# Optimization experiments

Hardware: AMD Instinct MI355X
Metric: run time of the kernel (lower is better)

Reference implementation:

```python
import jax, jax.numpy as jnp
import numpy as np

H = 4096        # hidden_size
NH = 32         # num query heads
NKV = 8         # num kv heads
HD = H // NH    # head_dim = 128
T_PREV = 16383  # cached tokens; new token makes T = 16384
BASE = 10000.0


def _rope(x, pos):
    # x: [heads, head_dim]; interleaved even/odd RoPE at a single position
    d = x.shape[-1]
    inv_freq = 1.0 / (BASE ** (jnp.arange(0, d, 2, dtype=jnp.float32) / d))
    f = pos * inv_freq                      # [d/2]
    c, s = jnp.cos(f), jnp.sin(f)
    xe, xo = x[..., 0::2], x[..., 1::2]
    out = jnp.stack([xe * c - xo * s, xe * s + xo * c], axis=-1)
    return out.reshape(x.shape)


def setup_inputs() -> dict:
    key = jax.random.key(0)
    ks = jax.random.split(key, 7)
    w = 0.02  # weight scale for numerical stability
    return {
        "hidden": jax.random.normal(ks[0], (H,), jnp.float32),
        "k_cache": jax.random.normal(ks[1], (T_PREV, NKV, HD), jnp.float32),
        "v_cache": jax.random.normal(ks[2], (T_PREV, NKV, HD), jnp.float32),
        "Wq": jax.random.normal(ks[3], (H, H), jnp.float32) * w,
        "Wk": jax.random.normal(ks[4], (NKV * HD, H), jnp.float32) * w,
        "Wv": jax.random.normal(ks[5], (NKV * HD, H), jnp.float32) * w,
        "Wo": jax.random.normal(ks[6], (H, H), jnp.float32) * w,
        "position_id": T_PREV,
    }


def reference(hidden, k_cache, v_cache, Wq, Wk, Wv, Wo, position_id):
    pos = jnp.float32(position_id)
    # projections (nn.Linear: y = W @ x), single token
    q = (Wq @ hidden).reshape(NH, HD)
    k = (Wk @ hidden).reshape(NKV, HD)
    v = (Wv @ hidden).reshape(NKV, HD)
    # inline RoPE on new q and k
    q = _rope(q, pos)
    k = _rope(k, pos)
    # contiguous KV including the new token
    k_all = jnp.concatenate([k_cache, k[None]], axis=0)   # [T, NKV, HD]
    v_all = jnp.concatenate([v_cache, v[None]], axis=0)
    # GQA: repeat KV heads to match query heads
    rep = NH // NKV
    k_all = jnp.repeat(k_all, rep, axis=1)                 # [T, NH, HD]
    v_all = jnp.repeat(v_all, rep, axis=1)
    # single-query attention
    scores = jnp.einsum('hd,thd->ht', q, k_all) / jnp.sqrt(jnp.float32(HD))
    attn = jax.nn.softmax(scores, axis=-1)                 # [NH, T]
    ctx = jnp.einsum('ht,thd->hd', attn, v_all)            # [NH, HD]
    # combine heads + output projection
    return Wo @ ctx.reshape(H)
```

## Files before the change

### kernel.cpp

```cpp
#include <hip/hip_runtime.h>
#include <math.h>

#define NH 32
#define NKV 8
#define HD 128
#define HDIM 4096
#define KVDIM 1024
#define TPREV 16383
#define NCHUNK 64
#define CHUNK 256

#define OFF_Q 0
#define OFF_K 4096
#define OFF_V 5120
#define OFF_PART 6144
#define PART_STRIDE 130
#define OFF_CTX (OFF_PART + NH * NCHUNK * PART_STRIDE)

__device__ __forceinline__ float wave_reduce_sum(float v) {
#pragma unroll
  for (int m = 32; m >= 1; m >>= 1) v += __shfl_xor(v, m, 64);
  return v;
}
__device__ __forceinline__ float wave_reduce_max(float v) {
#pragma unroll
  for (int m = 32; m >= 1; m >>= 1) v = fmaxf(v, __shfl_xor(v, m, 64));
  return v;
}
__device__ __forceinline__ float dot4(float4 a, float4 b) {
  return a.x * b.x + a.y * b.y + a.z * b.z + a.w * b.w;
}

__global__ __launch_bounds__(256) void qkv_rope_kernel(
    const float* __restrict__ Wq, const float* __restrict__ Wk,
    const float* __restrict__ Wv, const float* __restrict__ hidden,
    const int* __restrict__ pos_p, float* __restrict__ ws) {
  int r = blockIdx.x * 4 + (threadIdx.x >> 6);
  int lane = threadIdx.x & 63;
  const float* W;
  int wr;
  if (r < HDIM) {
    W = Wq; wr = r;
  } else if (r < HDIM + KVDIM) {
    W = Wk; wr = r - HDIM;
  } else {
    W = Wv; wr = r - HDIM - KVDIM;
  }
  const float4* w4 = (const float4*)(W + (size_t)wr * HDIM);
  const float4* h4 = (const float4*)hidden;
  float s = 0.f;
#pragma unroll
  for (int base = 0; base < 16; base += 8) {
    float4 a[8], b[8];
#pragma unroll
    for (int j = 0; j < 8; ++j) a[j] = w4[lane + 64 * (base + j)];
#pragma unroll
    for (int j = 0; j < 8; ++j) b[j] = h4[lane + 64 * (base + j)];
#pragma unroll
    for (int j = 0; j < 8; ++j) s += dot4(a[j], b[j]);
  }
  s = wave_reduce_sum(s);
  __shared__ float rs[4];
  if (lane == 0) rs[threadIdx.x >> 6] = s;
  __syncthreads();
  if (threadIdx.x < 2) {
    int r0 = blockIdx.x * 4 + (int)threadIdx.x * 2;
    float S0 = rs[threadIdx.x * 2], S1 = rs[threadIdx.x * 2 + 1];
    if (r0 < HDIM + KVDIM) {
      int j = (r0 & (HD - 1)) >> 1;
      double f = (double)(*pos_p) * pow(10000.0, -(double)j / 64.0);
      float c = (float)cos(f), sn = (float)sin(f);
      ws[r0] = S0 * c - S1 * sn;
      ws[r0 + 1] = S0 * sn + S1 * c;
    } else {
      ws[r0] = S0;
      ws[r0 + 1] = S1;
    }
  }
}

__global__ __launch_bounds__(256, 2) void attn_chunk_kernel(
    const float* __restrict__ k_cache, const float* __restrict__ v_cache,
    float* __restrict__ ws) {
  int g = blockIdx.x >> 6;
  int c = blockIdx.x & 63;
  int t0 = c * CHUNK;
  int tid = threadIdx.x;

  __shared__ float qs[4 * HD];
  __shared__ float sc[CHUNK * 5];
  __shared__ float vacc[8][4][HD];
  __shared__ float wredm[4][4], wredl[4][4];
  __shared__ float mh[4], lh[4];

  for (int i = tid; i < 4 * HD; i += 256) qs[i] = ws[OFF_Q + g * 4 * HD + i];
  __syncthreads();

  const float rscale = 0.08838834764831845f;

  int tok = t0 + tid;
  bool valid = tok < TPREV;
  float s0 = -1e30f, s1 = -1e30f, s2 = -1e30f, s3 = -1e30f;
  if (valid) {
    const float4* kp = (const float4*)(k_cache + (size_t)tok * KVDIM + g * HD);
    const float4* q4 = (const float4*)qs;
    s0 = 0.f; s1 = 0.f; s2 = 0.f; s3 = 0.f;
#pragma unroll
    for (int base = 0; base < 32; base += 8) {
      float4 kk[8];
#pragma unroll
      for (int j = 0; j < 8; ++j) kk[j] = kp[base + j];
#pragma unroll
      for (int j = 0; j < 8; ++j) {
        s0 += dot4(kk[j], q4[0 * 32 + base + j]);
        s1 += dot4(kk[j], q4[1 * 32 + base + j]);
        s2 += dot4(kk[j], q4[2 * 32 + base + j]);
        s3 += dot4(kk[j], q4[3 * 32 + base + j]);
      }
    }
    s0 *= rscale; s1 *= rscale; s2 *= rscale; s3 *= rscale;
  }

  float m0 = wave_reduce_max(s0), m1 = wave_reduce_max(s1);
  float m2 = wave_reduce_max(s2), m3 = wave_reduce_max(s3);
  if ((tid & 63) == 0) {
    int w = tid >> 6;
    wredm[w][0] = m0; wredm[w][1] = m1; wredm[w][2] = m2; wredm[w][3] = m3;
  }
  __syncthreads();
  if (tid < 4)
    mh[tid] = fmaxf(fmaxf(wredm[0][tid], wredm[1][tid]),
                    fmaxf(wredm[2][tid], wredm[3][tid]));
  __syncthreads();

  float e0 = expf(s0 - mh[0]), e1 = expf(s1 - mh[1]);
  float e2 = expf(s2 - mh[2]), e3 = expf(s3 - mh[3]);
  sc[tid * 5 + 0] = e0;
  sc[tid * 5 + 1] = e1;
  sc[tid * 5 + 2] = e2;
  sc[tid * 5 + 3] = e3;
  float l0 = wave_reduce_sum(e0), l1 = wave_reduce_sum(e1);
  float l2 = wave_reduce_sum(e2), l3 = wave_reduce_sum(e3);
  if ((tid & 63) == 0) {
    int w = tid >> 6;
    wredl[w][0] = l0; wredl[w][1] = l1; wredl[w][2] = l2; wredl[w][3] = l3;
  }
  __syncthreads();
  if (tid < 4)
    lh[tid] = wredl[0][tid] + wredl[1][tid] + wredl[2][tid] + wredl[3][tid];
  __syncthreads();

  int grp = tid >> 5, lane = tid & 31;
  float4 a0 = {0, 0, 0, 0}, a1 = {0, 0, 0, 0}, a2 = {0, 0, 0, 0},
         a3 = {0, 0, 0, 0};
  const float4 z4 = {0, 0, 0, 0};
#pragma unroll
  for (int base = 0; base < 32; base += 4) {
    float4 vv[4];
#pragma unroll
    for (int j = 0; j < 4; ++j) {
      int it = grp + 8 * (base + j);
      int t = t0 + it;
      vv[j] = (t < TPREV)
                  ? ((const float4*)(v_cache + (size_t)t * KVDIM + g * HD))[lane]
                  : z4;
    }
#pragma unroll
    for (int j = 0; j < 4; ++j) {
      int it = grp + 8 * (base + j);
      float p0 = sc[it * 5 + 0], p1 = sc[it * 5 + 1];
      float p2 = sc[it * 5 + 2], p3 = sc[it * 5 + 3];
      a0.x = fmaf(p0, vv[j].x, a0.x); a0.y = fmaf(p0, vv[j].y, a0.y);
      a0.z = fmaf(p0, vv[j].z, a0.z); a0.w = fmaf(p0, vv[j].w, a0.w);
      a1.x = fmaf(p1, vv[j].x, a1.x); a1.y = fmaf(p1, vv[j].y, a1.y);
      a1.z = fmaf(p1, vv[j].z, a1.z); a1.w = fmaf(p1, vv[j].w, a1.w);
      a2.x = fmaf(p2, vv[j].x, a2.x); a2.y = fmaf(p2, vv[j].y, a2.y);
      a2.z = fmaf(p2, vv[j].z, a2.z); a2.w = fmaf(p2, vv[j].w, a2.w);
      a3.x = fmaf(p3, vv[j].x, a3.x); a3.y = fmaf(p3, vv[j].y, a3.y);
      a3.z = fmaf(p3, vv[j].z, a3.z); a3.w = fmaf(p3, vv[j].w, a3.w);
    }
  }
  ((float4*)&vacc[grp][0][0])[lane] = a0;
  ((float4*)&vacc[grp][1][0])[lane] = a1;
  ((float4*)&vacc[grp][2][0])[lane] = a2;
  ((float4*)&vacc[grp][3][0])[lane] = a3;
  __syncthreads();

  float* part = ws + OFF_PART;
#pragma unroll
  for (int rep = 0; rep < 2; ++rep) {
    int p = tid + rep * 256;
    int h = p >> 7, d = p & 127;
    float s = 0.f;
#pragma unroll
    for (int g2 = 0; g2 < 8; ++g2) s += vacc[g2][h][d];
    part[(size_t)((g * 4 + h) * NCHUNK + c) * PART_STRIDE + d] = s;
  }
  if (tid < 4) {
    part[(size_t)((g * 4 + tid) * NCHUNK + c) * PART_STRIDE + 128] = mh[tid];
    part[(size_t)((g * 4 + tid) * NCHUNK + c) * PART_STRIDE + 129] = lh[tid];
  }
}

__global__ __launch_bounds__(256) void combine_kernel(float* __restrict__ ws) {
  int h = blockIdx.x;
  int g = h >> 2;
  int tid = threadIdx.x;
  const float rscale = 0.08838834764831845f;
  const float* ph = ws + OFF_PART + (size_t)h * NCHUNK * PART_STRIDE;

  __shared__ float red[HD];
  __shared__ float wexp[NCHUNK];
  __shared__ float Msh, Lsh;
  __shared__ float acc2[HD];

  if (tid < HD) red[tid] = ws[OFF_Q + h * HD + tid] * ws[OFF_K + g * HD + tid];
  __syncthreads();
#pragma unroll
  for (int s2 = 64; s2 >= 1; s2 >>= 1) {
    if (tid < s2 && tid + s2 < HD) red[tid] += red[tid + s2];
    __syncthreads();
  }
  float snew = red[0] * rscale;

  if (tid < 64) {
    float m = ph[tid * PART_STRIDE + 128];
    float M = wave_reduce_max(fmaxf(m, snew));
    float w = expf(m - M);
    float lp = ph[tid * PART_STRIDE + 129] * w;
    float L = wave_reduce_sum(lp);
    wexp[tid] = w;
    if (tid == 0) { Msh = M; Lsh = L; }
  }
  __syncthreads();
  float M = Msh;
  float en = expf(snew - M);
  float L = Lsh + en;

  int half = tid >> 7, d = tid & 127;
  float acc = 0.f;
  int cbeg = half * 32;
#pragma unroll 8
  for (int c2 = cbeg; c2 < cbeg + 32; ++c2)
    acc = fmaf(ph[(size_t)c2 * PART_STRIDE + d], wexp[c2], acc);
  if (half == 0) acc2[d] = acc;
  __syncthreads();
  if (half == 1) acc2[d] += acc;
  __syncthreads();
  if (tid < HD)
    ws[OFF_CTX + h * HD + tid] =
        (acc2[tid] + en * ws[OFF_V + g * HD + tid]) / L;
}

__global__ __launch_bounds__(256) void out_matvec_kernel(
    const float* __restrict__ Wo, const float* __restrict__ ws,
    float* __restrict__ out) {
  int r = blockIdx.x * 4 + (threadIdx.x >> 6);
  int lane = threadIdx.x & 63;
  const float4* w4 = (const float4*)(Wo + (size_t)r * HDIM);
  const float4* x4 = (const float4*)(ws + OFF_CTX);
  float s = 0.f;
#pragma unroll
  for (int base = 0; base < 16; base += 8) {
    float4 a[8], b[8];
#pragma unroll
    for (int j = 0; j < 8; ++j) a[j] = w4[lane + 64 * (base + j)];
#pragma unroll
    for (int j = 0; j < 8; ++j) b[j] = x4[lane + 64 * (base + j)];
#pragma unroll
    for (int j = 0; j < 8; ++j) s += dot4(a[j], b[j]);
  }
  s = wave_reduce_sum(s);
  if (lane == 0) out[r] = s;
}

extern "C" void kernel_launch(void* const* d_in, const int* in_sizes, int n_in,
                              void* d_out, int out_size, void* d_ws,
                              size_t ws_size, hipStream_t stream) {
  const float* hidden = (const float*)d_in[0];
  const float* k_cache = (const float*)d_in[1];
  const float* v_cache = (const float*)d_in[2];
  const float* Wq = (const float*)d_in[3];
  const float* Wk = (const float*)d_in[4];
  const float* Wv = (const float*)d_in[5];
  const float* Wo = (const float*)d_in[6];
  const int* pos = (const int*)d_in[7];
  float* out = (float*)d_out;
  float* ws = (float*)d_ws;

  qkv_rope_kernel<<<(HDIM + 2 * KVDIM) / 4, 256, 0, stream>>>(Wq, Wk, Wv,
                                                              hidden, pos, ws);
  attn_chunk_kernel<<<NKV * NCHUNK, 256, 0, stream>>>(k_cache, v_cache, ws);
  combine_kernel<<<NH, 256, 0, stream>>>(ws);
  out_matvec_kernel<<<HDIM / 4, 256, 0, stream>>>(Wo, ws, out);
}
```

Measured before the change: 286.8 us.

## Halve attention chunk size, split K dot across thread pairs, cheapen RoPE trig

Doubles the number of attention chunks (128 tokens each), so the grid covers more CUs. Each K row's dot product is now split across two threads that combine with a lane shuffle. Occupancy is raised via launch bounds, and the combine kernel is generalised to reduce 128 partials across four waves. The RoPE frequency computation replaces double pow/cos/sin with a bitwise product of precomputed powers plus range reduction and float sincos. In exchange, the partials workspace and the combine kernel's work both double.

```diff
diff --git a/kernel.cpp b/kernel.cpp
--- a/kernel.cpp
+++ b/kernel.cpp
@@ -7,8 +7,8 @@
 #define HDIM 4096
 #define KVDIM 1024
 #define TPREV 16383
-#define NCHUNK 64
-#define CHUNK 256
+#define NCHUNK 128
+#define CHUNK 128
 
 #define OFF_Q 0
 #define OFF_K 4096
@@ -68,8 +68,18 @@
     float S0 = rs[threadIdx.x * 2], S1 = rs[threadIdx.x * 2 + 1];
     if (r0 < HDIM + KVDIM) {
       int j = (r0 & (HD - 1)) >> 1;
-      double f = (double)(*pos_p) * pow(10000.0, -(double)j / 64.0);
-      float c = (float)cos(f), sn = (float)sin(f);
+      double lowp = 1.0;
+      if (j & 1) lowp *= 0.8659643233600653;
+      if (j & 2) lowp *= 0.7498942093324559;
+      if (j & 4) lowp *= 0.5623413251903491;
+      if (j & 8) lowp *= 0.31622776601683794;
+      double hi = (j & 16) ? 0.1 : 1.0;
+      if (j & 32) hi *= 0.01;
+      double f = (double)(*pos_p) * (lowp * hi);
+      double k2 = floor(f * 0.15915494309189535);
+      double rr = f - k2 * 6.283185307179586;
+      float fr = (float)rr;
+      float c = cosf(fr), sn = sinf(fr);
       ws[r0] = S0 * c - S1 * sn;
       ws[r0 + 1] = S0 * sn + S1 * c;
     } else {
@@ -79,11 +89,11 @@
   }
 }
 
-__global__ __launch_bounds__(256, 2) void attn_chunk_kernel(
+__global__ __launch_bounds__(256, 4) void attn_chunk_kernel(
     const float* __restrict__ k_cache, const float* __restrict__ v_cache,
     float* __restrict__ ws) {
-  int g = blockIdx.x >> 6;
-  int c = blockIdx.x & 63;
+  int g = blockIdx.x >> 7;
+  int c = blockIdx.x & 127;
   int t0 = c * CHUNK;
   int tid = threadIdx.x;
 
@@ -98,28 +108,36 @@
 
   const float rscale = 0.08838834764831845f;
 
-  int tok = t0 + tid;
+  int itok = tid >> 1;
+  int hf = tid & 1;
+  int tok = t0 + itok;
   bool valid = tok < TPREV;
   float s0 = -1e30f, s1 = -1e30f, s2 = -1e30f, s3 = -1e30f;
   if (valid) {
-    const float4* kp = (const float4*)(k_cache + (size_t)tok * KVDIM + g * HD);
+    const float4* kp =
+        (const float4*)(k_cache + (size_t)tok * KVDIM + g * HD + hf * 64);
     const float4* q4 = (const float4*)qs;
     s0 = 0.f; s1 = 0.f; s2 = 0.f; s3 = 0.f;
 #pragma unroll
-    for (int base = 0; base < 32; base += 8) {
+    for (int base = 0; base < 16; base += 8) {
       float4 kk[8];
 #pragma unroll
       for (int j = 0; j < 8; ++j) kk[j] = kp[base + j];
 #pragma unroll
       for (int j = 0; j < 8; ++j) {
-        s0 += dot4(kk[j], q4[0 * 32 + base + j]);
-        s1 += dot4(kk[j], q4[1 * 32 + base + j]);
-        s2 += dot4(kk[j], q4[2 * 32 + base + j]);
-        s3 += dot4(kk[j], q4[3 * 32 + base + j]);
+        int qi = hf * 16 + base + j;
+        s0 += dot4(kk[j], q4[0 * 32 + qi]);
+        s1 += dot4(kk[j], q4[1 * 32 + qi]);
+        s2 += dot4(kk[j], q4[2 * 32 + qi]);
+        s3 += dot4(kk[j], q4[3 * 32 + qi]);
       }
     }
-    s0 *= rscale; s1 *= rscale; s2 *= rscale; s3 *= rscale;
-  }
+  }
+  s0 += __shfl_xor(s0, 1, 64);
+  s1 += __shfl_xor(s1, 1, 64);
+  s2 += __shfl_xor(s2, 1, 64);
+  s3 += __shfl_xor(s3, 1, 64);
+  s0 *= rscale; s1 *= rscale; s2 *= rscale; s3 *= rscale;
 
   float m0 = wave_reduce_max(s0), m1 = wave_reduce_max(s1);
   float m2 = wave_reduce_max(s2), m3 = wave_reduce_max(s3);
@@ -135,12 +153,14 @@
 
   float e0 = expf(s0 - mh[0]), e1 = expf(s1 - mh[1]);
   float e2 = expf(s2 - mh[2]), e3 = expf(s3 - mh[3]);
-  sc[tid * 5 + 0] = e0;
-  sc[tid * 5 + 1] = e1;
-  sc[tid * 5 + 2] = e2;
-  sc[tid * 5 + 3] = e3;
-  float l0 = wave_reduce_sum(e0), l1 = wave_reduce_sum(e1);
-  float l2 = wave_reduce_sum(e2), l3 = wave_reduce_sum(e3);
+  if (hf == 0) {
+    sc[itok * 5 + 0] = e0;
+    sc[itok * 5 + 1] = e1;
+    sc[itok * 5 + 2] = e2;
+    sc[itok * 5 + 3] = e3;
+  }
+  float l0 = 0.5f * wave_reduce_sum(e0), l1 = 0.5f * wave_reduce_sum(e1);
+  float l2 = 0.5f * wave_reduce_sum(e2), l3 = 0.5f * wave_reduce_sum(e3);
   if ((tid & 63) == 0) {
     int w = tid >> 6;
     wredl[w][0] = l0; wredl[w][1] = l1; wredl[w][2] = l2; wredl[w][3] = l3;
@@ -155,7 +175,7 @@
          a3 = {0, 0, 0, 0};
   const float4 z4 = {0, 0, 0, 0};
 #pragma unroll
-  for (int base = 0; base < 32; base += 4) {
+  for (int base = 0; base < 16; base += 4) {
     float4 vv[4];
 #pragma unroll
     for (int j = 0; j < 4; ++j) {
@@ -211,7 +231,7 @@
 
   __shared__ float red[HD];
   __shared__ float wexp[NCHUNK];
-  __shared__ float Msh, Lsh;
+  __shared__ float wm[4], wl[4];
   __shared__ float acc2[HD];
 
   if (tid < HD) red[tid] = ws[OFF_Q + h * HD + tid] * ws[OFF_K + g * HD + tid];
@@ -223,25 +243,25 @@
   }
   float snew = red[0] * rscale;
 
-  if (tid < 64) {
-    float m = ph[tid * PART_STRIDE + 128];
-    float M = wave_reduce_max(fmaxf(m, snew));
-    float w = expf(m - M);
-    float lp = ph[tid * PART_STRIDE + 129] * w;
-    float L = wave_reduce_sum(lp);
-    wexp[tid] = w;
-    if (tid == 0) { Msh = M; Lsh = L; }
-  }
-  __syncthreads();
-  float M = Msh;
+  float mv = (tid < NCHUNK) ? ph[(size_t)tid * PART_STRIDE + 128] : -1e30f;
+  float lv = (tid < NCHUNK) ? ph[(size_t)tid * PART_STRIDE + 129] : 0.f;
+  float mw = wave_reduce_max(mv);
+  if ((tid & 63) == 0) wm[tid >> 6] = mw;
+  __syncthreads();
+  float M = fmaxf(fmaxf(fmaxf(wm[0], wm[1]), fmaxf(wm[2], wm[3])), snew);
+  float w = expf(mv - M);
+  if (tid < NCHUNK) wexp[tid] = w;
+  float lw = wave_reduce_sum(lv * w);
+  if ((tid & 63) == 0) wl[tid >> 6] = lw;
+  __syncthreads();
   float en = expf(snew - M);
-  float L = Lsh + en;
+  float L = wl[0] + wl[1] + wl[2] + wl[3] + en;
 
   int half = tid >> 7, d = tid & 127;
   float acc = 0.f;
-  int cbeg = half * 32;
+  int cbeg = half * (NCHUNK / 2);
 #pragma unroll 8
-  for (int c2 = cbeg; c2 < cbeg + 32; ++c2)
+  for (int c2 = cbeg; c2 < cbeg + NCHUNK / 2; ++c2)
     acc = fmaf(ph[(size_t)c2 * PART_STRIDE + d], wexp[c2], acc);
   if (half == 0) acc2[d] = acc;
   __syncthreads();
```

After: 292.8 us. 1.02x slower.
